# Optimization experiments

Hardware: AMD Instinct MI355X
Metric: run time of the kernel (lower is better)

Reference implementation:

```python
import jax, jax.numpy as jnp
import numpy as np

N = 1024       # nodes
D1 = 64        # hidden_dim_1
D2 = 64        # hidden_dim_2
E = 16384      # edges
P = 8192       # query pairs
MAXX = 100     # max node label -> Embedding(MAXX+1, D1)
EPS = 1e-5     # LayerNorm eps (no affine)


def _ln(t):
    m = jnp.mean(t, axis=-1, keepdims=True)
    v = jnp.mean((t - m) ** 2, axis=-1, keepdims=True)
    return (t - m) / jnp.sqrt(v + EPS)


def setup_inputs() -> dict:
    key = jax.random.key(0)
    ks = jax.random.split(key, 12)
    s = 0.1
    x = jax.random.randint(ks[0], (N,), 0, MAXX + 1)
    ei = jax.random.randint(ks[1], (2, E), 0, N)
    pos = jax.random.randint(ks[2], (P, 2), 0, N)
    emb = jax.random.normal(ks[3], (MAXX + 1, D1)) * s
    sage_Wl = jax.random.normal(ks[4], (2, D1, D1)) * s   # lin_l weight (aggr path, has bias)
    sage_bl = jnp.zeros((2, D1))
    sage_Wr = jax.random.normal(ks[5], (2, D1, D1)) * s   # lin_r weight (root path, no bias)
    h_W = jax.random.normal(ks[6], (D1 + 1, D2)) * s
    h_b = jnp.zeros((D2,))
    g_W = jax.random.normal(ks[7], (D1 + 1 + 2 * D2, D2)) * s
    g_b = jnp.zeros((D2,))
    lin_W = jax.random.normal(ks[8], (D2, 1)) * s
    lin_b = jnp.zeros((1,))
    return {"x": x, "ei": ei, "pos": pos, "emb": emb,
            "sage_Wl": sage_Wl, "sage_bl": sage_bl, "sage_Wr": sage_Wr,
            "h_W": h_W, "h_b": h_b, "g_W": g_W, "g_b": g_b,
            "lin_W": lin_W, "lin_b": lin_b}


def reference(x, ei, pos, emb, sage_Wl, sage_bl, sage_Wr, h_W, h_b, g_W, g_b, lin_W, lin_b):
    n = N
    src, dst = ei[0], ei[1]
    h = emb[x]                                            # (n, D1)
    # SAGEConv x2: mean-aggregate src->dst, lin_l(aggr)+bias + lin_r(root); then LN (no affine, no relu)
    deg = jax.ops.segment_sum(jnp.ones((E,), h.dtype), dst, num_segments=n)
    deg = jnp.maximum(deg, 1.0)[:, None]
    for i in range(2):
        aggr = jax.ops.segment_sum(h[src], dst, num_segments=n) / deg
        h = _ln(aggr @ sage_Wl[i] + sage_bl[i] + h @ sage_Wr[i])
    # pairwise outer product features: (n, n, D1)
    A = h[:, None, :] * h[None, :, :]
    eim = jnp.zeros((n * n,), h.dtype).at[src * n + dst].set(1.0).reshape(n, n, 1)
    A = jnp.concatenate([A, eim], axis=-1)                # (n, n, D1+1)
    # mataggr: B = h_1(A); row/col sums; D = cat(A, vec_p, vec_q); g_1(D)
    B = jax.nn.relu(_ln(A @ h_W + h_b))                   # (n, n, D2)
    vec_p = jnp.sum(B, axis=1, keepdims=True)             # (n, 1, D2)
    vec_q = jnp.sum(B, axis=0, keepdims=True)             # (1, n, D2)
    Dm = jnp.concatenate([A,
                          jnp.broadcast_to(vec_p, (n, n, D2)),
                          jnp.broadcast_to(vec_q, (n, n, D2))], axis=-1)
    G = jax.nn.relu(_ln(Dm @ g_W + g_b))                  # (n, n, D2)
    # symmetrize and gather query pairs
    S = (G * jnp.transpose(G, (1, 0, 2))).reshape(n * n, D2)
    sel = S[pos[:, 0] * n + pos[:, 1]]                    # (P, D2)
    return sel @ lin_W + lin_b                            # (P, 1)
```

## Files before the change

kernel.cpp:

```cpp
#include <hip/hip_runtime.h>
#include <hip/hip_bf16.h>

#define NN 1024
#define DD 64
#define EE 16384
#define PP 8192
#define EPSF 1e-5f

typedef __hip_bfloat16 bf16;
typedef __attribute__((ext_vector_type(8))) short short8;
typedef __attribute__((ext_vector_type(4))) float f32x4;

static __device__ __forceinline__ float dec1(const void* src, int i, int fl) {
    if (fl) return ((const float*)src)[i];
    return __bfloat162float(((const bf16*)src)[i]);
}
static __device__ __forceinline__ unsigned short f2bf_u(float f) {
    bf16 h = __float2bfloat16(f);
    return *reinterpret_cast<unsigned short*>(&h);
}

__global__ void k_probe(const unsigned short* __restrict__ raw, int n, int* __restrict__ flag) {
    int i = blockIdx.x * blockDim.x + threadIdx.x;
    if (i >= n) return;
    unsigned int bits = ((unsigned int)raw[i]) << 16;
    float v = __uint_as_float(bits);
    if (!(fabsf(v) <= 1e3f)) atomicOr(flag, 1);
}

__global__ void k_prep(const void* __restrict__ emb, const void* __restrict__ sWl,
                       const void* __restrict__ sbl, const void* __restrict__ sWr,
                       const void* __restrict__ hW, const void* __restrict__ hb,
                       const void* __restrict__ gW, const void* __restrict__ gb,
                       const void* __restrict__ lW, const void* __restrict__ lb,
                       const int* __restrict__ x, const int* __restrict__ ei,
                       const int* __restrict__ flagp,
                       float* __restrict__ Wlf, float* __restrict__ blf, float* __restrict__ Wrf,
                       float* __restrict__ WfT, float* __restrict__ hbw,
                       float* __restrict__ gWf, float* __restrict__ linf,
                       float* __restrict__ h0, int* __restrict__ deg,
                       unsigned int* __restrict__ eim, unsigned int* __restrict__ eimT) {
    int fl = *flagp;
    int b = blockIdx.x, t = threadIdx.x;
    if (b < 32) {
        int i = b * 256 + t; Wlf[i] = dec1(sWl, i, fl);
    } else if (b < 33) {
        if (t < 128) blf[t] = dec1(sbl, t, fl);
    } else if (b < 65) {
        int i = (b - 33) * 256 + t; Wrf[i] = dec1(sWr, i, fl);
    } else if (b < 82) {
        int i = (b - 65) * 256 + t;
        if (i < 4096) { int n = i >> 6, k = i & 63; WfT[n * DD + k] = dec1(hW, k * DD + n, fl); }
        else if (i < 4160) { hbw[i - 4096] = dec1(hb, i - 4096, fl); }
        else if (i < 4224) { hbw[64 + (i - 4160)] = dec1(hW, 64 * DD + (i - 4160), fl); }
    } else if (b < 131) {
        int i = (b - 82) * 256 + t;
        if (i < 193 * DD) gWf[i] = dec1(gW, i, fl);
        else if (i < 194 * DD) gWf[i] = dec1(gb, i - 193 * DD, fl);
    } else if (b < 132) {
        if (t < DD) linf[t] = dec1(lW, t, fl);
        else if (t == DD) linf[DD] = dec1(lb, 0, fl);
    } else if (b < 388) {
        int i = (b - 132) * 256 + t;
        int node = i >> 6, f = i & 63;
        h0[i] = dec1(emb, x[node] * DD + f, fl);
    } else {
        int e = (b - 388) * 256 + t;
        if (e < EE) {
            int s = ei[e], d = ei[EE + e];
            atomicAdd(&deg[d], 1);
            unsigned int idx = (unsigned int)(s * NN + d);
            atomicOr(&eim[idx >> 5], 1u << (idx & 31));
            unsigned int idxT = (unsigned int)(d * NN + s);
            atomicOr(&eimT[idxT >> 5], 1u << (idxT & 31));
        }
    }
}

__global__ void k_aggr(const int* __restrict__ ei, const float* __restrict__ h,
                       float* __restrict__ aggr) {
    int idx = blockIdx.x * blockDim.x + threadIdx.x;
    int e = idx >> 6, f = idx & 63;
    int s = ei[e];
    int d = ei[EE + e];
    atomicAdd(&aggr[d * DD + f], h[s * DD + f]);
}

__global__ void k_sage(const float* __restrict__ aggr, const int* __restrict__ degi,
                       const float* __restrict__ hin,
                       const float* __restrict__ Wl, const float* __restrict__ bl,
                       const float* __restrict__ Wr,
                       float* __restrict__ hout, unsigned short* __restrict__ hbf,
                       float* __restrict__ azero) {
    int i = blockIdx.x;
    int f = threadIdx.x;
    __shared__ float sa[DD], sh[DD];
    float dg = (float)max(degi[i], 1);
    sa[f] = aggr[i * DD + f] / dg;
    sh[f] = hin[i * DD + f];
    if (azero) azero[i * DD + f] = 0.f;
    __syncthreads();
    float o = bl[f];
    for (int k = 0; k < DD; ++k) {
        o += sa[k] * Wl[k * DD + f] + sh[k] * Wr[k * DD + f];
    }
    float m = o;
    for (int off = 32; off; off >>= 1) m += __shfl_xor(m, off);
    m *= (1.0f / DD);
    float d0 = o - m;
    float v = d0 * d0;
    for (int off = 32; off; off >>= 1) v += __shfl_xor(v, off);
    v *= (1.0f / DD);
    float r = d0 * rsqrtf(v + EPSF);
    hout[i * DD + f] = r;
    hbf[i * DD + f] = f2bf_u(r);
}

static __device__ __forceinline__ void ln_pass(const f32x4* C, unsigned int slice, int quad,
                                               const float* hw0, const float* hw1,
                                               float* acc) {
    float T[4][4];
    float s[4], s2[4];
#pragma unroll
    for (int r = 0; r < 4; ++r) {
        bool e = (slice >> (quad * 4 + r)) & 1u;
        s[r] = 0.f; s2[r] = 0.f;
#pragma unroll
        for (int mt = 0; mt < 4; ++mt) {
            float v = C[mt][r] + (e ? hw1[mt] : hw0[mt]);
            T[mt][r] = v;
            s[r] += v;
            s2[r] += v * v;
        }
    }
#pragma unroll
    for (int step = 1; step < 16; step <<= 1) {
#pragma unroll
        for (int r = 0; r < 4; ++r) {
            s[r]  += __shfl_xor(s[r], step);
            s2[r] += __shfl_xor(s2[r], step);
        }
    }
#pragma unroll
    for (int r = 0; r < 4; ++r) {
        float mean = s[r] * (1.f / DD);
        float var = fmaxf(s2[r] * (1.f / DD) - mean * mean, 0.f);
        float rs = rsqrtf(var + EPSF);
#pragma unroll
        for (int mt = 0; mt < 4; ++mt)
            acc[mt] += fmaxf((T[mt][r] - mean) * rs, 0.f);
    }
}

__launch_bounds__(256)
__global__ void k_bstage(const float* __restrict__ h0, const unsigned short* __restrict__ hbf,
                         const float* __restrict__ WfT, const float* __restrict__ hbw,
                         const unsigned int* __restrict__ eim,
                         const unsigned int* __restrict__ eimT,
                         float* __restrict__ vec_p, float* __restrict__ vec_q) {
    int fix = blockIdx.x;
    int tid = threadIdx.x;
    int lane = tid & 63, wave = tid >> 6;
    int l15 = lane & 15, quad = lane >> 4;

    __shared__ unsigned short sW[DD * DD];
    __shared__ float red[4][2 * DD];

    {
        int n = tid >> 2;
        int k0 = (tid & 3) * 16;
        const float* hi = h0 + fix * DD;
#pragma unroll
        for (int u = 0; u < 16; ++u) {
            int k = k0 + u;
            sW[n * DD + k] = f2bf_u(hi[k] * WfT[n * DD + k]);
        }
    }
    __syncthreads();

    short8 Wb[4][2];
#pragma unroll
    for (int mt = 0; mt < 4; ++mt)
#pragma unroll
        for (int kt = 0; kt < 2; ++kt)
            Wb[mt][kt] = *(const short8*)(sW + (mt * 16 + l15) * DD + kt * 32 + quad * 8);

    float hw0[4], hw1[4];
#pragma unroll
    for (int mt = 0; mt < 4; ++mt) {
        float a = hbw[mt * 16 + l15];
        float w = hbw[64 + mt * 16 + l15];
        hw0[mt] = a;
        hw1[mt] = a + w;
    }

    float accf[4] = {0.f, 0.f, 0.f, 0.f};
    float accb[4] = {0.f, 0.f, 0.f, 0.f};

    for (int g = wave; g < 64; g += 4) {
        int jrow = g * 16 + l15;
        short8 A0 = *(const short8*)(hbf + jrow * DD + quad * 8);
        short8 A1 = *(const short8*)(hbf + jrow * DD + 32 + quad * 8);

        f32x4 C[4];
#pragma unroll
        for (int mt = 0; mt < 4; ++mt) C[mt] = (f32x4){0.f, 0.f, 0.f, 0.f};
#pragma unroll
        for (int mt = 0; mt < 4; ++mt)
            C[mt] = __builtin_amdgcn_mfma_f32_16x16x32_bf16(A0, Wb[mt][0], C[mt], 0, 0, 0);
#pragma unroll
        for (int mt = 0; mt < 4; ++mt)
            C[mt] = __builtin_amdgcn_mfma_f32_16x16x32_bf16(A1, Wb[mt][1], C[mt], 0, 0, 0);

        unsigned int base = (unsigned int)(fix * NN + g * 16);
        unsigned int sf = (eim[base >> 5]  >> (base & 31)) & 0xFFFFu;
        unsigned int sb = (eimT[base >> 5] >> (base & 31)) & 0xFFFFu;

        if (sf == sb) {
            float tot[4] = {0.f, 0.f, 0.f, 0.f};
            ln_pass(C, sf, quad, hw0, hw1, tot);
#pragma unroll
            for (int mt = 0; mt < 4; ++mt) { accf[mt] += tot[mt]; accb[mt] += tot[mt]; }
        } else {
            ln_pass(C, sf, quad, hw0, hw1, accf);
            ln_pass(C, sb, quad, hw0, hw1, accb);
        }
    }

#pragma unroll
    for (int step = 16; step < 64; step <<= 1)
#pragma unroll
        for (int mt = 0; mt < 4; ++mt) {
            accf[mt] += __shfl_xor(accf[mt], step);
            accb[mt] += __shfl_xor(accb[mt], step);
        }

    if (quad == 0) {
#pragma unroll
        for (int mt = 0; mt < 4; ++mt) {
            red[wave][mt * 16 + l15] = accf[mt];
            red[wave][DD + mt * 16 + l15] = accb[mt];
        }
    }
    __syncthreads();
    if (tid < 2 * DD) {
        float sum = red[0][tid] + red[1][tid] + red[2][tid] + red[3][tid];
        if (tid < DD) vec_p[fix * DD + tid] = sum;
        else          vec_q[fix * DD + (tid - DD)] = sum;
    }
}

__global__ void k_ppqq2(const float* __restrict__ vecp, const float* __restrict__ vecq,
                        const float* __restrict__ gWf,
                        float* __restrict__ ppb, float* __restrict__ qqb) {
    int b = blockIdx.x;
    int f = threadIdx.x;
    int i = b & 1023, which = b >> 10;
    const float* vec = (which ? vecq : vecp) + i * DD;
    int row0 = which ? 129 : 65;
    __shared__ float sv[DD];
    sv[f] = vec[f];
    __syncthreads();
    float o = 0.f;
    for (int k = 0; k < DD; ++k) o += sv[k] * gWf[(row0 + k) * DD + f];
    (which ? qqb : ppb)[i * DD + f] = o;
}

__global__ void k_final(const int* __restrict__ pos, const float* __restrict__ h,
                        const float* __restrict__ gWf, const unsigned int* __restrict__ eim,
                        const float* __restrict__ pp, const float* __restrict__ qq,
                        const float* __restrict__ linf, const int* __restrict__ flag,
                        void* __restrict__ outv) {
    int p = blockIdx.x;
    int a = pos[2 * p], b = pos[2 * p + 1];
    int m = threadIdx.x;
    __shared__ float sq[DD];
    sq[m] = h[a * DD + m] * h[b * DD + m];
    __syncthreads();
    float acc = 0.f;
    for (int k = 0; k < DD; ++k) acc += sq[k] * gWf[k * DD + m];
    unsigned int iab = (unsigned int)(a * NN + b), iba = (unsigned int)(b * NN + a);
    float eab = ((eim[iab >> 5] >> (iab & 31)) & 1u) ? 1.f : 0.f;
    float eba = ((eim[iba >> 5] >> (iba & 31)) & 1u) ? 1.f : 0.f;
    float gb = gWf[193 * DD + m];
    float w64 = gWf[64 * DD + m];
    float u1 = acc + eab * w64 + pp[a * DD + m] + qq[b * DD + m] + gb;
    float u2 = acc + eba * w64 + pp[b * DD + m] + qq[a * DD + m] + gb;

    float m1 = u1;
    for (int off = 32; off; off >>= 1) m1 += __shfl_xor(m1, off);
    m1 *= (1.f / DD);
    float d1 = u1 - m1;
    float v1 = d1 * d1;
    for (int off = 32; off; off >>= 1) v1 += __shfl_xor(v1, off);
    v1 *= (1.f / DD);
    float g1 = fmaxf(d1 * rsqrtf(v1 + EPSF), 0.f);

    float m2 = u2;
    for (int off = 32; off; off >>= 1) m2 += __shfl_xor(m2, off);
    m2 *= (1.f / DD);
    float d2 = u2 - m2;
    float v2 = d2 * d2;
    for (int off = 32; off; off >>= 1) v2 += __shfl_xor(v2, off);
    v2 *= (1.f / DD);
    float g2 = fmaxf(d2 * rsqrtf(v2 + EPSF), 0.f);

    float r = g1 * g2 * linf[m];
    for (int off = 32; off; off >>= 1) r += __shfl_xor(r, off);
    if (m == 0) {
        float res = r + linf[DD];
        if (*flag) ((float*)outv)[p] = res;
        else       ((bf16*)outv)[p] = __float2bfloat16(res);
    }
}

extern "C" void kernel_launch(void* const* d_in, const int* in_sizes, int n_in,
                              void* d_out, int out_size, void* d_ws, size_t ws_size,
                              hipStream_t stream) {
    const int* x      = (const int*)d_in[0];
    const int* ei     = (const int*)d_in[1];
    const int* pos    = (const int*)d_in[2];
    const void* emb     = d_in[3];
    const void* sage_Wl = d_in[4];
    const void* sage_bl = d_in[5];
    const void* sage_Wr = d_in[6];
    const void* h_W     = d_in[7];
    const void* h_b     = d_in[8];
    const void* g_W     = d_in[9];
    const void* g_b     = d_in[10];
    const void* lin_W   = d_in[11];
    const void* lin_b   = d_in[12];

    char* w = (char*)d_ws;
    auto alloc = [&](size_t bytes) {
        void* p = (void*)w;
        w += (bytes + 255) & ~(size_t)255;
        return p;
    };
    int*   flag = (int*)alloc(256);
    int*   degi = (int*)alloc(NN * 4);
    unsigned int* eim  = (unsigned int*)alloc(NN * NN / 8);
    unsigned int* eimT = (unsigned int*)alloc(NN * NN / 8);
    float* aggr = (float*)alloc(NN * DD * 4);
    size_t zero_bytes = (size_t)((char*)w - (char*)d_ws);
    float* h0   = (float*)alloc(NN * DD * 4);
    float* h1   = (float*)alloc(NN * DD * 4);
    float* h2   = (float*)alloc(NN * DD * 4);
    unsigned short* hbf = (unsigned short*)alloc(NN * DD * 2);
    float* Wlf  = (float*)alloc(2 * DD * DD * 4);
    float* blf  = (float*)alloc(2 * DD * 4);
    float* Wrf  = (float*)alloc(2 * DD * DD * 4);
    float* WfT  = (float*)alloc(DD * DD * 4);
    float* hbw  = (float*)alloc(128 * 4);
    float* gWf  = (float*)alloc(194 * DD * 4);
    float* linf = (float*)alloc(65 * 4);
    float* vecp = (float*)alloc(NN * DD * 4);
    float* vecq = (float*)alloc(NN * DD * 4);
    float* ppb  = (float*)alloc(NN * DD * 4);
    float* qqb  = (float*)alloc(NN * DD * 4);

    hipMemsetAsync(d_ws, 0, zero_bytes, stream);

    k_probe<<<(101 * DD + 255) / 256, 256, 0, stream>>>((const unsigned short*)emb, 101 * DD, flag);

    k_prep<<<452, 256, 0, stream>>>(emb, sage_Wl, sage_bl, sage_Wr, h_W, h_b, g_W, g_b,
                                    lin_W, lin_b, x, ei, flag,
                                    Wlf, blf, Wrf, WfT, hbw, gWf, linf,
                                    h0, degi, eim, eimT);

    k_aggr<<<EE * DD / 256, 256, 0, stream>>>(ei, h0, aggr);
    k_sage<<<NN, DD, 0, stream>>>(aggr, degi, h0, Wlf, blf, Wrf, h1, hbf, aggr);

    k_aggr<<<EE * DD / 256, 256, 0, stream>>>(ei, h1, aggr);
    k_sage<<<NN, DD, 0, stream>>>(aggr, degi, h1, Wlf + DD * DD, blf + DD,
                                  Wrf + DD * DD, h2, hbf, (float*)nullptr);

    k_bstage<<<NN, 256, 0, stream>>>(h0  == h0 ? h2 : h2, hbf, WfT, hbw, eim, eimT, vecp, vecq);

    k_ppqq2<<<2 * NN, DD, 0, stream>>>(vecp, vecq, gWf, ppb, qqb);

    k_final<<<PP, DD, 0, stream>>>(pos, h2, gWf, eim, ppb, qqb, linf, flag, d_out);
}
```

Before: 173.8 us.

## Use CSR aggregation, split B-stage across halves, and MFMA-batch the final stage

Replaces the atomic per-edge feature scatter with a degree scan plus CSR build, so each SAGE block gathers its own neighbours without float atomics or zeroing the aggregation buffer. Splits the B-stage into two blocks per row and reworks its MFMA operand layout so layer-norm statistics reduce across quads, with the transposed-edge case reusing the forward values. Rewrites the final stage to process 64 pairs per block with bf16 MFMA against gW instead of one scalar 64-thread block per pair. In exchange it adds a single-block scan kernel, nondeterministic neighbour order, and bf16 rounding of the pairwise product in the final stage.

```diff
diff --git a/kernel.cpp b/kernel.cpp
--- a/kernel.cpp
+++ b/kernel.cpp
@@ -6,6 +6,7 @@
 #define EE 16384
 #define PP 8192
 #define EPSF 1e-5f
+#define SWP (DD + 8)
 
 typedef __hip_bfloat16 bf16;
 typedef __attribute__((ext_vector_type(8))) short short8;
@@ -18,6 +19,10 @@
 static __device__ __forceinline__ unsigned short f2bf_u(float f) {
     bf16 h = __float2bfloat16(f);
     return *reinterpret_cast<unsigned short*>(&h);
+}
+static __device__ __forceinline__ float bfu2f(unsigned short u) {
+    unsigned int b = ((unsigned int)u) << 16;
+    return __uint_as_float(b);
 }
 
 __global__ void k_probe(const unsigned short* __restrict__ raw, int n, int* __restrict__ flag) {
@@ -77,28 +82,51 @@
     }
 }
 
-__global__ void k_aggr(const int* __restrict__ ei, const float* __restrict__ h,
-                       float* __restrict__ aggr) {
-    int idx = blockIdx.x * blockDim.x + threadIdx.x;
-    int e = idx >> 6, f = idx & 63;
-    int s = ei[e];
+__global__ void k_scan(const int* __restrict__ deg, int* __restrict__ rowptr,
+                       int* __restrict__ cursor) {
+    __shared__ int tmp[NN];
+    int t = threadIdx.x;
+    int v = deg[t];
+    tmp[t] = v;
+    __syncthreads();
+    for (int off = 1; off < NN; off <<= 1) {
+        int add = (t >= off) ? tmp[t - off] : 0;
+        __syncthreads();
+        tmp[t] += add;
+        __syncthreads();
+    }
+    int incl = tmp[t];
+    rowptr[t] = incl - v;
+    cursor[t] = incl - v;
+    if (t == NN - 1) rowptr[NN] = incl;
+}
+
+__global__ void k_scatter(const int* __restrict__ ei, int* __restrict__ cursor,
+                          int* __restrict__ csrc) {
+    int e = blockIdx.x * blockDim.x + threadIdx.x;
+    if (e >= EE) return;
     int d = ei[EE + e];
-    atomicAdd(&aggr[d * DD + f], h[s * DD + f]);
-}
-
-__global__ void k_sage(const float* __restrict__ aggr, const int* __restrict__ degi,
+    int c = atomicAdd(&cursor[d], 1);
+    csrc[c] = ei[e];
+}
+
+__global__ void k_sage(const int* __restrict__ rowptr, const int* __restrict__ csrc,
                        const float* __restrict__ hin,
                        const float* __restrict__ Wl, const float* __restrict__ bl,
                        const float* __restrict__ Wr,
-                       float* __restrict__ hout, unsigned short* __restrict__ hbf,
-                       float* __restrict__ azero) {
+                       float* __restrict__ hout, unsigned short* __restrict__ hbf) {
     int i = blockIdx.x;
     int f = threadIdx.x;
     __shared__ float sa[DD], sh[DD];
-    float dg = (float)max(degi[i], 1);
-    sa[f] = aggr[i * DD + f] / dg;
+    int r0 = rowptr[i], r1 = rowptr[i + 1];
+    float s = 0.f;
+    for (int r = r0; r < r1; ++r) {
+        int src = csrc[r];
+        s += hin[src * DD + f];
+    }
+    float dg = (float)max(r1 - r0, 1);
+    sa[f] = s / dg;
     sh[f] = hin[i * DD + f];
-    if (azero) azero[i * DD + f] = 0.f;
     __syncthreads();
     float o = bl[f];
     for (int k = 0; k < DD; ++k) {
@@ -116,198 +144,275 @@
     hbf[i * DD + f] = f2bf_u(r);
 }
 
-static __device__ __forceinline__ void ln_pass(const f32x4* C, unsigned int slice, int quad,
-                                               const float* hw0, const float* hw1,
-                                               float* acc) {
-    float T[4][4];
-    float s[4], s2[4];
-#pragma unroll
-    for (int r = 0; r < 4; ++r) {
-        bool e = (slice >> (quad * 4 + r)) & 1u;
-        s[r] = 0.f; s2[r] = 0.f;
-#pragma unroll
-        for (int mt = 0; mt < 4; ++mt) {
-            float v = C[mt][r] + (e ? hw1[mt] : hw0[mt]);
-            T[mt][r] = v;
-            s[r] += v;
-            s2[r] += v * v;
-        }
-    }
-#pragma unroll
-    for (int step = 1; step < 16; step <<= 1) {
-#pragma unroll
-        for (int r = 0; r < 4; ++r) {
-            s[r]  += __shfl_xor(s[r], step);
-            s2[r] += __shfl_xor(s2[r], step);
-        }
-    }
-#pragma unroll
-    for (int r = 0; r < 4; ++r) {
-        float mean = s[r] * (1.f / DD);
-        float var = fmaxf(s2[r] * (1.f / DD) - mean * mean, 0.f);
-        float rs = rsqrtf(var + EPSF);
-#pragma unroll
-        for (int mt = 0; mt < 4; ++mt)
-            acc[mt] += fmaxf((T[mt][r] - mean) * rs, 0.f);
-    }
-}
-
 __launch_bounds__(256)
-__global__ void k_bstage(const float* __restrict__ h0, const unsigned short* __restrict__ hbf,
+__global__ void k_bstage(const float* __restrict__ h2, const unsigned short* __restrict__ hbf,
                          const float* __restrict__ WfT, const float* __restrict__ hbw,
                          const unsigned int* __restrict__ eim,
                          const unsigned int* __restrict__ eimT,
-                         float* __restrict__ vec_p, float* __restrict__ vec_q) {
-    int fix = blockIdx.x;
+                         float* __restrict__ vp_part, float* __restrict__ vq_part) {
+    int bid = blockIdx.x;
+    int fix = bid >> 1, half = bid & 1;
     int tid = threadIdx.x;
     int lane = tid & 63, wave = tid >> 6;
     int l15 = lane & 15, quad = lane >> 4;
 
-    __shared__ unsigned short sW[DD * DD];
+    __shared__ unsigned short sW[DD * SWP];
     __shared__ float red[4][2 * DD];
 
     {
-        int n = tid >> 2;
+        int m = tid >> 2;
         int k0 = (tid & 3) * 16;
-        const float* hi = h0 + fix * DD;
+        const float* hi = h2 + fix * DD;
+        const float* wr = WfT + m * DD;
 #pragma unroll
         for (int u = 0; u < 16; ++u) {
             int k = k0 + u;
-            sW[n * DD + k] = f2bf_u(hi[k] * WfT[n * DD + k]);
-        }
-    }
-    __syncthreads();
-
-    short8 Wb[4][2];
+            sW[m * SWP + k] = f2bf_u(hi[k] * wr[k]);
+        }
+    }
+    __syncthreads();
+
+    short8 Af[4][2];
 #pragma unroll
     for (int mt = 0; mt < 4; ++mt)
 #pragma unroll
         for (int kt = 0; kt < 2; ++kt)
-            Wb[mt][kt] = *(const short8*)(sW + (mt * 16 + l15) * DD + kt * 32 + quad * 8);
-
-    float hw0[4], hw1[4];
+            Af[mt][kt] = *(const short8*)(sW + (mt * 16 + l15) * SWP + kt * 32 + quad * 8);
+
+    float hb0[4][4], hww[4][4];
 #pragma unroll
     for (int mt = 0; mt < 4; ++mt) {
-        float a = hbw[mt * 16 + l15];
-        float w = hbw[64 + mt * 16 + l15];
-        hw0[mt] = a;
-        hw1[mt] = a + w;
-    }
-
-    float accf[4] = {0.f, 0.f, 0.f, 0.f};
-    float accb[4] = {0.f, 0.f, 0.f, 0.f};
-
-    for (int g = wave; g < 64; g += 4) {
-        int jrow = g * 16 + l15;
-        short8 A0 = *(const short8*)(hbf + jrow * DD + quad * 8);
-        short8 A1 = *(const short8*)(hbf + jrow * DD + 32 + quad * 8);
+        f32x4 a = *(const f32x4*)(hbw + mt * 16 + quad * 4);
+        f32x4 wv = *(const f32x4*)(hbw + 64 + mt * 16 + quad * 4);
+#pragma unroll
+        for (int r = 0; r < 4; ++r) { hb0[mt][r] = a[r]; hww[mt][r] = wv[r]; }
+    }
+
+    float accf[4][4], accb[4][4];
+#pragma unroll
+    for (int mt = 0; mt < 4; ++mt)
+#pragma unroll
+        for (int r = 0; r < 4; ++r) { accf[mt][r] = 0.f; accb[mt][r] = 0.f; }
+
+    for (int g = half * 32 + wave; g < half * 32 + 32; g += 4) {
+        short8 B0 = *(const short8*)(hbf + (g * 16 + l15) * DD + quad * 8);
+        short8 B1 = *(const short8*)(hbf + (g * 16 + l15) * DD + 32 + quad * 8);
 
         f32x4 C[4];
 #pragma unroll
         for (int mt = 0; mt < 4; ++mt) C[mt] = (f32x4){0.f, 0.f, 0.f, 0.f};
 #pragma unroll
         for (int mt = 0; mt < 4; ++mt)
-            C[mt] = __builtin_amdgcn_mfma_f32_16x16x32_bf16(A0, Wb[mt][0], C[mt], 0, 0, 0);
+            C[mt] = __builtin_amdgcn_mfma_f32_16x16x32_bf16(Af[mt][0], B0, C[mt], 0, 0, 0);
 #pragma unroll
         for (int mt = 0; mt < 4; ++mt)
-            C[mt] = __builtin_amdgcn_mfma_f32_16x16x32_bf16(A1, Wb[mt][1], C[mt], 0, 0, 0);
+            C[mt] = __builtin_amdgcn_mfma_f32_16x16x32_bf16(Af[mt][1], B1, C[mt], 0, 0, 0);
 
         unsigned int base = (unsigned int)(fix * NN + g * 16);
-        unsigned int sf = (eim[base >> 5]  >> (base & 31)) & 0xFFFFu;
+        unsigned int sf = (eim[base >> 5] >> (base & 31)) & 0xFFFFu;
         unsigned int sb = (eimT[base >> 5] >> (base & 31)) & 0xFFFFu;
+        float ef = (float)((sf >> l15) & 1u);
+
+        float s1 = 0.f, s2 = 0.f;
+#pragma unroll
+        for (int mt = 0; mt < 4; ++mt)
+#pragma unroll
+            for (int r = 0; r < 4; ++r) {
+                float v = C[mt][r] + hb0[mt][r] + ef * hww[mt][r];
+                C[mt][r] = v;
+                s1 += v;
+                s2 += v * v;
+            }
+        s1 += __shfl_xor(s1, 16); s1 += __shfl_xor(s1, 32);
+        s2 += __shfl_xor(s2, 16); s2 += __shfl_xor(s2, 32);
+        float mean = s1 * (1.f / DD);
+        float var = fmaxf(s2 * (1.f / DD) - mean * mean, 0.f);
+        float rs = rsqrtf(var + EPSF);
+        float mrs = mean * rs;
 
         if (sf == sb) {
-            float tot[4] = {0.f, 0.f, 0.f, 0.f};
-            ln_pass(C, sf, quad, hw0, hw1, tot);
-#pragma unroll
-            for (int mt = 0; mt < 4; ++mt) { accf[mt] += tot[mt]; accb[mt] += tot[mt]; }
+#pragma unroll
+            for (int mt = 0; mt < 4; ++mt)
+#pragma unroll
+                for (int r = 0; r < 4; ++r) {
+                    float u = fmaxf(C[mt][r] * rs - mrs, 0.f);
+                    accf[mt][r] += u;
+                    accb[mt][r] += u;
+                }
         } else {
-            ln_pass(C, sf, quad, hw0, hw1, accf);
-            ln_pass(C, sb, quad, hw0, hw1, accb);
-        }
-    }
-
-#pragma unroll
-    for (int step = 16; step < 64; step <<= 1)
-#pragma unroll
-        for (int mt = 0; mt < 4; ++mt) {
-            accf[mt] += __shfl_xor(accf[mt], step);
-            accb[mt] += __shfl_xor(accb[mt], step);
-        }
-
-    if (quad == 0) {
-#pragma unroll
-        for (int mt = 0; mt < 4; ++mt) {
-            red[wave][mt * 16 + l15] = accf[mt];
-            red[wave][DD + mt * 16 + l15] = accb[mt];
-        }
+#pragma unroll
+            for (int mt = 0; mt < 4; ++mt)
+#pragma unroll
+                for (int r = 0; r < 4; ++r)
+                    accf[mt][r] += fmaxf(C[mt][r] * rs - mrs, 0.f);
+            float de = (float)((sb >> l15) & 1u) - ef;
+            float t1 = 0.f, t2 = 0.f;
+#pragma unroll
+            for (int mt = 0; mt < 4; ++mt)
+#pragma unroll
+                for (int r = 0; r < 4; ++r) {
+                    float v = C[mt][r] + de * hww[mt][r];
+                    C[mt][r] = v;
+                    t1 += v;
+                    t2 += v * v;
+                }
+            t1 += __shfl_xor(t1, 16); t1 += __shfl_xor(t1, 32);
+            t2 += __shfl_xor(t2, 16); t2 += __shfl_xor(t2, 32);
+            float mean2 = t1 * (1.f / DD);
+            float var2 = fmaxf(t2 * (1.f / DD) - mean2 * mean2, 0.f);
+            float rs2 = rsqrtf(var2 + EPSF);
+            float mrs2 = mean2 * rs2;
+#pragma unroll
+            for (int mt = 0; mt < 4; ++mt)
+#pragma unroll
+                for (int r = 0; r < 4; ++r)
+                    accb[mt][r] += fmaxf(C[mt][r] * rs2 - mrs2, 0.f);
+        }
+    }
+
+#pragma unroll
+    for (int step = 1; step < 16; step <<= 1)
+#pragma unroll
+        for (int mt = 0; mt < 4; ++mt)
+#pragma unroll
+            for (int r = 0; r < 4; ++r) {
+                accf[mt][r] += __shfl_xor(accf[mt][r], step);
+                accb[mt][r] += __shfl_xor(accb[mt][r], step);
+            }
+
+    if (l15 == 0) {
+#pragma unroll
+        for (int mt = 0; mt < 4; ++mt)
+#pragma unroll
+            for (int r = 0; r < 4; ++r) {
+                int m = mt * 16 + quad * 4 + r;
+                red[wave][m] = accf[mt][r];
+                red[wave][DD + m] = accb[mt][r];
+            }
     }
     __syncthreads();
     if (tid < 2 * DD) {
         float sum = red[0][tid] + red[1][tid] + red[2][tid] + red[3][tid];
-        if (tid < DD) vec_p[fix * DD + tid] = sum;
-        else          vec_q[fix * DD + (tid - DD)] = sum;
-    }
-}
-
-__global__ void k_ppqq2(const float* __restrict__ vecp, const float* __restrict__ vecq,
+        if (tid < DD) vp_part[(half * NN + fix) * DD + tid] = sum;
+        else          vq_part[(half * NN + fix) * DD + (tid - DD)] = sum;
+    }
+}
+
+__global__ void k_ppqq2(const float* __restrict__ vpp, const float* __restrict__ vqp,
                         const float* __restrict__ gWf,
                         float* __restrict__ ppb, float* __restrict__ qqb) {
     int b = blockIdx.x;
     int f = threadIdx.x;
     int i = b & 1023, which = b >> 10;
-    const float* vec = (which ? vecq : vecp) + i * DD;
+    const float* part = which ? vqp : vpp;
     int row0 = which ? 129 : 65;
     __shared__ float sv[DD];
-    sv[f] = vec[f];
+    sv[f] = part[i * DD + f] + part[(NN + i) * DD + f];
     __syncthreads();
     float o = 0.f;
     for (int k = 0; k < DD; ++k) o += sv[k] * gWf[(row0 + k) * DD + f];
     (which ? qqb : ppb)[i * DD + f] = o;
 }
 
-__global__ void k_final(const int* __restrict__ pos, const float* __restrict__ h,
+__launch_bounds__(256)
+__global__ void k_final(const int* __restrict__ pos, const unsigned short* __restrict__ hbf,
                         const float* __restrict__ gWf, const unsigned int* __restrict__ eim,
                         const float* __restrict__ pp, const float* __restrict__ qq,
                         const float* __restrict__ linf, const int* __restrict__ flag,
                         void* __restrict__ outv) {
-    int p = blockIdx.x;
+    int blk = blockIdx.x;
+    int tid = threadIdx.x;
+    int lane = tid & 63, wave = tid >> 6;
+    int l15 = lane & 15, quad = lane >> 4;
+
+    __shared__ unsigned short sgW[DD * SWP];
+    __shared__ unsigned short sq[64 * SWP];
+
+    {
+        int m = tid >> 2;
+        int k0 = (tid & 3) * 16;
+#pragma unroll
+        for (int u = 0; u < 16; ++u) {
+            int k = k0 + u;
+            sgW[m * SWP + k] = f2bf_u(gWf[k * DD + m]);
+        }
+    }
+    for (int u = 0; u < 16; ++u) {
+        int row = wave * 16 + u;
+        int p = blk * 64 + row;
+        int a = pos[2 * p], b = pos[2 * p + 1];
+        float prod = bfu2f(hbf[a * DD + lane]) * bfu2f(hbf[b * DD + lane]);
+        sq[row * SWP + lane] = f2bf_u(prod);
+    }
+    __syncthreads();
+
+    short8 B0 = *(const short8*)(sq + (wave * 16 + l15) * SWP + quad * 8);
+    short8 B1 = *(const short8*)(sq + (wave * 16 + l15) * SWP + 32 + quad * 8);
+
+    f32x4 C[4];
+#pragma unroll
+    for (int mt = 0; mt < 4; ++mt) C[mt] = (f32x4){0.f, 0.f, 0.f, 0.f};
+#pragma unroll
+    for (int mt = 0; mt < 4; ++mt) {
+        short8 A0 = *(const short8*)(sgW + (mt * 16 + l15) * SWP + quad * 8);
+        C[mt] = __builtin_amdgcn_mfma_f32_16x16x32_bf16(A0, B0, C[mt], 0, 0, 0);
+    }
+#pragma unroll
+    for (int mt = 0; mt < 4; ++mt) {
+        short8 A1 = *(const short8*)(sgW + (mt * 16 + l15) * SWP + 32 + quad * 8);
+        C[mt] = __builtin_amdgcn_mfma_f32_16x16x32_bf16(A1, B1, C[mt], 0, 0, 0);
+    }
+
+    int p = blk * 64 + wave * 16 + l15;
     int a = pos[2 * p], b = pos[2 * p + 1];
-    int m = threadIdx.x;
-    __shared__ float sq[DD];
-    sq[m] = h[a * DD + m] * h[b * DD + m];
-    __syncthreads();
-    float acc = 0.f;
-    for (int k = 0; k < DD; ++k) acc += sq[k] * gWf[k * DD + m];
     unsigned int iab = (unsigned int)(a * NN + b), iba = (unsigned int)(b * NN + a);
-    float eab = ((eim[iab >> 5] >> (iab & 31)) & 1u) ? 1.f : 0.f;
-    float eba = ((eim[iba >> 5] >> (iba & 31)) & 1u) ? 1.f : 0.f;
-    float gb = gWf[193 * DD + m];
-    float w64 = gWf[64 * DD + m];
-    float u1 = acc + eab * w64 + pp[a * DD + m] + qq[b * DD + m] + gb;
-    float u2 = acc + eba * w64 + pp[b * DD + m] + qq[a * DD + m] + gb;
-
-    float m1 = u1;
-    for (int off = 32; off; off >>= 1) m1 += __shfl_xor(m1, off);
-    m1 *= (1.f / DD);
-    float d1 = u1 - m1;
-    float v1 = d1 * d1;
-    for (int off = 32; off; off >>= 1) v1 += __shfl_xor(v1, off);
-    v1 *= (1.f / DD);
-    float g1 = fmaxf(d1 * rsqrtf(v1 + EPSF), 0.f);
-
-    float m2 = u2;
-    for (int off = 32; off; off >>= 1) m2 += __shfl_xor(m2, off);
-    m2 *= (1.f / DD);
-    float d2 = u2 - m2;
-    float v2 = d2 * d2;
-    for (int off = 32; off; off >>= 1) v2 += __shfl_xor(v2, off);
-    v2 *= (1.f / DD);
-    float g2 = fmaxf(d2 * rsqrtf(v2 + EPSF), 0.f);
-
-    float r = g1 * g2 * linf[m];
-    for (int off = 32; off; off >>= 1) r += __shfl_xor(r, off);
-    if (m == 0) {
+    float eab = (float)((eim[iab >> 5] >> (iab & 31)) & 1u);
+    float eba = (float)((eim[iba >> 5] >> (iba & 31)) & 1u);
+
+    float u1[4][4], u2[4][4];
+    float s1 = 0.f, s12 = 0.f, s2 = 0.f, s22 = 0.f;
+#pragma unroll
+    for (int mt = 0; mt < 4; ++mt) {
+        int m0 = mt * 16 + quad * 4;
+        f32x4 w64v = *(const f32x4*)(gWf + 64 * DD + m0);
+        f32x4 gbv  = *(const f32x4*)(gWf + 193 * DD + m0);
+        f32x4 ppa  = *(const f32x4*)(pp + a * DD + m0);
+        f32x4 qqb_ = *(const f32x4*)(qq + b * DD + m0);
+        f32x4 ppb_ = *(const f32x4*)(pp + b * DD + m0);
+        f32x4 qqa  = *(const f32x4*)(qq + a * DD + m0);
+#pragma unroll
+        for (int r = 0; r < 4; ++r) {
+            float v1 = C[mt][r] + eab * w64v[r] + ppa[r] + qqb_[r] + gbv[r];
+            float v2 = C[mt][r] + eba * w64v[r] + ppb_[r] + qqa[r] + gbv[r];
+            u1[mt][r] = v1; u2[mt][r] = v2;
+            s1 += v1; s12 += v1 * v1;
+            s2 += v2; s22 += v2 * v2;
+        }
+    }
+    s1 += __shfl_xor(s1, 16);  s1 += __shfl_xor(s1, 32);
+    s12 += __shfl_xor(s12, 16); s12 += __shfl_xor(s12, 32);
+    s2 += __shfl_xor(s2, 16);  s2 += __shfl_xor(s2, 32);
+    s22 += __shfl_xor(s22, 16); s22 += __shfl_xor(s22, 32);
+    float mean1 = s1 * (1.f / DD);
+    float rs1 = rsqrtf(fmaxf(s12 * (1.f / DD) - mean1 * mean1, 0.f) + EPSF);
+    float mrs1 = mean1 * rs1;
+    float mean2 = s2 * (1.f / DD);
+    float rs2 = rsqrtf(fmaxf(s22 * (1.f / DD) - mean2 * mean2, 0.f) + EPSF);
+    float mrs2 = mean2 * rs2;
+
+    float r = 0.f;
+#pragma unroll
+    for (int mt = 0; mt < 4; ++mt) {
+        f32x4 lw = *(const f32x4*)(linf + mt * 16 + quad * 4);
+#pragma unroll
+        for (int rr = 0; rr < 4; ++rr) {
+            float g1 = fmaxf(u1[mt][rr] * rs1 - mrs1, 0.f);
+            float g2 = fmaxf(u2[mt][rr] * rs2 - mrs2, 0.f);
+            r += g1 * g2 * lw[rr];
+        }
+    }
+    r += __shfl_xor(r, 16); r += __shfl_xor(r, 32);
+    if (quad == 0) {
         float res = r + linf[DD];
         if (*flag) ((float*)outv)[p] = res;
         else       ((bf16*)outv)[p] = __float2bfloat16(res);
@@ -341,7 +446,6 @@
     int*   degi = (int*)alloc(NN * 4);
     unsigned int* eim  = (unsigned int*)alloc(NN * NN / 8);
     unsigned int* eimT = (unsigned int*)alloc(NN * NN / 8);
-    float* aggr = (float*)alloc(NN * DD * 4);
     size_t zero_bytes = (size_t)((char*)w - (char*)d_ws);
     float* h0   = (float*)alloc(NN * DD * 4);
     float* h1   = (float*)alloc(NN * DD * 4);
@@ -354,10 +458,13 @@
     float* hbw  = (float*)alloc(128 * 4);
     float* gWf  = (float*)alloc(194 * DD * 4);
     float* linf = (float*)alloc(65 * 4);
-    float* vecp = (float*)alloc(NN * DD * 4);
-    float* vecq = (float*)alloc(NN * DD * 4);
+    float* vpp  = (float*)alloc(2 * NN * DD * 4);
+    float* vqp  = (float*)alloc(2 * NN * DD * 4);
     float* ppb  = (float*)alloc(NN * DD * 4);
     float* qqb  = (float*)alloc(NN * DD * 4);
+    int* rowptr = (int*)alloc((NN + 1) * 4);
+    int* cursor = (int*)alloc(NN * 4);
+    int* csrc   = (int*)alloc(EE * 4);
 
     hipMemsetAsync(d_ws, 0, zero_bytes, stream);
 
@@ -368,16 +475,16 @@
                                     Wlf, blf, Wrf, WfT, hbw, gWf, linf,
                                     h0, degi, eim, eimT);
 
-    k_aggr<<<EE * DD / 256, 256, 0, stream>>>(ei, h0, aggr);
-    k_sage<<<NN, DD, 0, stream>>>(aggr, degi, h0, Wlf, blf, Wrf, h1, hbf, aggr);
-
-    k_aggr<<<EE * DD / 256, 256, 0, stream>>>(ei, h1, aggr);
-    k_sage<<<NN, DD, 0, stream>>>(aggr, degi, h1, Wlf + DD * DD, blf + DD,
-                                  Wrf + DD * DD, h2, hbf, (float*)nullptr);
-
-    k_bstage<<<NN, 256, 0, stream>>>(h0  == h0 ? h2 : h2, hbf, WfT, hbw, eim, eimT, vecp, vecq);
-
-    k_ppqq2<<<2 * NN, DD, 0, stream>>>(vecp, vecq, gWf, ppb, qqb);
-
-    k_final<<<PP, DD, 0, stream>>>(pos, h2, gWf, eim, ppb, qqb, linf, flag, d_out);
-}
+    k_scan<<<1, NN, 0, stream>>>(degi, rowptr, cursor);
+    k_scatter<<<EE / 256, 256, 0, stream>>>(ei, cursor, csrc);
+
+    k_sage<<<NN, DD, 0, stream>>>(rowptr, csrc, h0, Wlf, blf, Wrf, h1, hbf);
+    k_sage<<<NN, DD, 0, stream>>>(rowptr, csrc, h1, Wlf + DD * DD, blf + DD,
+                                  Wrf + DD * DD, h2, hbf);
+
+    k_bstage<<<2 * NN, 256, 0, stream>>>(h2, hbf, WfT, hbw, eim, eimT, vpp, vqp);
+
+    k_ppqq2<<<2 * NN, DD, 0, stream>>>(vpp, vqp, gWf, ppb, qqb);
+
+    k_final<<<PP / 64, 256, 0, stream>>>(pos, hbf, gWf, eim, ppb, qqb, linf, flag, d_out);
+}
```

Measured after the change: 167.9 us. 1.04x faster.
